# Kernel tuning notes

Measured on AMD Instinct MI355X. Metric: run time of the kernel, lower is better.

## Reference

```python
import jax, jax.numpy as jnp
import numpy as np

TOP_K = 2


def setup_inputs() -> dict:
    key = jax.random.key(0)
    ks = jax.random.split(key, 5)
    B, S, D, F, E = 2, 2048, 1024, 3584, 8
    scale_in = 1.0 / np.sqrt(D)
    scale_f = 1.0 / np.sqrt(F)
    return {
        "hidden_states": jax.random.normal(ks[0], (B, S, D), dtype=jnp.float32),
        "gate_w": jax.random.normal(ks[1], (E, D), dtype=jnp.float32) * scale_in,
        "w1": jax.random.normal(ks[2], (E, F, D), dtype=jnp.float32) * scale_in,
        "w3": jax.random.normal(ks[3], (E, F, D), dtype=jnp.float32) * scale_in,
        "w2": jax.random.normal(ks[4], (E, D, F), dtype=jnp.float32) * scale_f,
    }


def _routing_weights(logits):
    # softmax over experts, select top-k, renormalize (Mixtral semantics)
    probs = jax.nn.softmax(logits, axis=-1)          # [T, E]
    topv, topi = jax.lax.top_k(probs, TOP_K)          # [T, k]
    topv = topv / jnp.sum(topv, axis=-1, keepdims=True)
    T, E = logits.shape
    w = jnp.zeros((T, E), dtype=logits.dtype)
    w = w.at[jnp.arange(T)[:, None], topi].set(topv)  # dense [T, E] routing weights
    return w


def reference(hidden_states, gate_w, w1, w3, w2):
    B, S, D = hidden_states.shape
    x = hidden_states.reshape(-1, D)                  # [T, D]
    logits = x @ gate_w.T                             # [T, E]
    rw = _routing_weights(logits)                     # [T, E]
    E = gate_w.shape[0]
    out = jnp.zeros_like(x)
    for e in range(E):                                # fixed small expert count
        h = jax.nn.silu(x @ w1[e].T) * (x @ w3[e].T)  # [T, F]
        out = out + rw[:, e:e + 1] * (h @ w2[e].T)    # [T, D]
    return out.reshape(B, S, D)
```

## Files before the change

### kernel.cpp

```cpp
#include <hip/hip_runtime.h>
#include <hip/hip_bf16.h>


#define T_TOK 4096
#define DIM   1024
#define FF    3584
#define NE    8
#define BM    128
#define CAP   (T_TOK*2 + NE*BM)

#define OFF_TOPI   256UL
#define OFF_TOPW   33024UL
#define OFF_TOKPOS 65792UL
#define OFF_ROWTOK 98560UL
#define OFF_XB     135424UL
#define OFF_BIG    8524032UL
#define OFF_W2B    OFF_BIG
#define OFF_RES    (OFF_BIG + 58720256UL)
#define OFF_H      (OFF_BIG + 117440512UL)
#define WS_NEED    (OFF_H + 66060288UL)

using f32x4 = __attribute__((ext_vector_type(4))) float;
using s16x8 = __attribute__((ext_vector_type(8))) short;

__device__ __forceinline__ ushort f2b(float f) {
    __hip_bfloat16 b = __float2bfloat16(f);
    ushort u; __builtin_memcpy(&u, &b, 2); return u;
}
__device__ __forceinline__ float blo(uint u){ u <<= 16; float f; __builtin_memcpy(&f,&u,4); return f; }
__device__ __forceinline__ float bhi(uint u){ u &= 0xFFFF0000u; float f; __builtin_memcpy(&f,&u,4); return f; }

__device__ __forceinline__ void gl_lds16(const ushort* g, ushort* l) {
    __builtin_amdgcn_global_load_lds(
        (const __attribute__((address_space(1))) void*)g,
        (__attribute__((address_space(3))) void*)l, 16, 0, 0);
}
__device__ __forceinline__ uint4 pack8(float4 v0, float4 v1) {
    uint4 o;
    o.x = f2b(v0.x) | ((uint)f2b(v0.y) << 16);
    o.y = f2b(v0.z) | ((uint)f2b(v0.w) << 16);
    o.z = f2b(v1.x) | ((uint)f2b(v1.y) << 16);
    o.w = f2b(v1.z) | ((uint)f2b(v1.w) << 16);
    return o;
}

#define LGKM0 do { asm volatile("s_waitcnt lgkmcnt(0)" ::: "memory"); \
                   __builtin_amdgcn_sched_barrier(0); } while (0)
#define VMC(n) asm volatile("s_waitcnt vmcnt(" #n ")" ::: "memory")
#define BAR()  __builtin_amdgcn_s_barrier()

__global__ __launch_bounds__(256)
void k_route(const float* __restrict__ x, const float* __restrict__ gw,
             int* __restrict__ topi, float* __restrict__ topw, int* __restrict__ counts)
{
    __shared__ float gws[NE*DIM];
    const int tid = threadIdx.x;
    for (int i = tid; i < NE*DIM/4; i += 256)
        ((float4*)gws)[i] = ((const float4*)gw)[i];
    __syncthreads();

    const int lane = tid & 63, wid = tid >> 6;
    const int t = blockIdx.x*4 + wid;

    float4 xr[4];
    const float4* xrow = (const float4*)(x + (size_t)t*DIM) + lane*4;
    #pragma unroll
    for (int i = 0; i < 4; ++i) xr[i] = xrow[i];

    float lg[NE];
    #pragma unroll
    for (int e = 0; e < NE; ++e) {
        const float4* g4 = (const float4*)(gws + e*DIM) + lane*4;
        float s = 0.f;
        #pragma unroll
        for (int i = 0; i < 4; ++i) {
            float4 g = g4[i];
            s += xr[i].x*g.x + xr[i].y*g.y + xr[i].z*g.z + xr[i].w*g.w;
        }
        #pragma unroll
        for (int off = 32; off; off >>= 1) s += __shfl_xor(s, off);
        lg[e] = s;
    }
    if (lane == 0) {
        float b1 = -1e30f, b2 = -1e30f; int i1 = 0, i2 = 0;
        #pragma unroll
        for (int e = 0; e < NE; ++e) {
            float v = lg[e];
            if (v > b1)      { b2 = b1; i2 = i1; b1 = v; i1 = e; }
            else if (v > b2) { b2 = v; i2 = e; }
        }
        float p2 = __expf(b2 - b1);
        float inv = 1.f / (1.f + p2);
        topi[2*t]   = i1; topi[2*t+1] = i2;
        topw[2*t]   = inv; topw[2*t+1] = p2*inv;
        atomicAdd(&counts[i1], 1); atomicAdd(&counts[i2], 1);
    }
}

__global__ void k_scan(const int* __restrict__ counts, int* __restrict__ offs,
                       int* __restrict__ rowTok)
{
    if (threadIdx.x == 0) {
        int acc = 0; offs[0] = 0;
        for (int e = 0; e < NE; ++e) {
            int p = (counts[e] + BM - 1) & ~(BM - 1);
            acc += p; offs[e+1] = acc;
        }
    }
    for (int i = threadIdx.x; i < CAP; i += blockDim.x) rowTok[i] = -1;
}

__global__ __launch_bounds__(256)
void k_scatter(const int* __restrict__ topi,
               const int* __restrict__ offs, int* __restrict__ cursor,
               int* __restrict__ rowTok, int* __restrict__ tokPos)
{
    int t = blockIdx.x*256 + threadIdx.x;
    #pragma unroll
    for (int j = 0; j < 2; ++j) {
        int e = topi[2*t + j];
        int pos = offs[e] + atomicAdd(&cursor[e], 1);
        rowTok[pos] = t;
        tokPos[2*t + j] = pos;
    }
}

__global__ __launch_bounds__(256)
void k_cvt(const float* __restrict__ src, ushort* __restrict__ dst)
{
    size_t i = (size_t)blockIdx.x*256 + threadIdx.x;
    float4 v0 = ((const float4*)src)[2*i], v1 = ((const float4*)src)[2*i+1];
    ((uint4*)dst)[i] = pack8(v0, v1);
}

__global__ __launch_bounds__(256)
void k_cvt13(const float* __restrict__ w1, const float* __restrict__ w3,
             ushort* __restrict__ w13)
{
    int i = blockIdx.x*256 + threadIdx.x;
    int k8 = i & 127;
    int rd = i >> 7;
    int e   = rd / 7168;
    int rem = rd - e*7168;
    int pb  = rem >> 9;
    int sc  = rem & 511;
    int g = sc >> 6, half = (sc >> 5) & 1, c = sc & 31;
    int f = pb*256 + g*32 + c;
    const float* src = (half ? w3 : w1) + ((size_t)e*FF + f)*DIM + k8*8;
    float4 v0 = ((const float4*)src)[0], v1 = ((const float4*)src)[1];
    ((uint4*)w13)[i] = pack8(v0, v1);
}

__global__ __launch_bounds__(512)
void k_gemm1(const ushort* __restrict__ xb, const ushort* __restrict__ w13,
             const int* __restrict__ offs, const int* __restrict__ rowTok,
             ushort* __restrict__ hout)
{
    __shared__ __align__(16) ushort As[3][128*32];
    __shared__ __align__(16) ushort Bs[3][512*32];
    const int rowStart = blockIdx.y * BM;
    if (rowStart >= offs[8]) return;
    int e = 0;
    #pragma unroll
    for (int k = 1; k < NE; ++k) if (rowStart >= offs[k]) e = k;
    const int pb = blockIdx.x;
    const ushort* __restrict__ Wb = w13 + ((size_t)(e*14 + pb)) * 512 * DIM;

    const int tid = threadIdx.x;
    const int lane = tid & 63, wid = tid >> 6;
    const int lo = lane & 15, hi = lane >> 4;

    const int srow = tid >> 2;
    const int q    = tid & 3;
    const int sig  = (tid >> 3) & 3;
    int tokS = rowTok[rowStart + srow]; if (tokS < 0) tokS = 0;
    const ushort* aS = xb + (size_t)tokS*DIM + (q ^ sig)*8;
    const ushort* bS = Wb + (size_t)srow*DIM + (q ^ sig)*8;

    const int sig2  = (lo >> 1) & 3;
    const int rdA   = lo*32 + ((hi ^ sig2) * 8);
    const int rdB   = (wid*64 + lo)*32 + ((hi ^ sig2) * 8);

    f32x4 acc[8][4];
    #pragma unroll
    for (int m = 0; m < 8; ++m)
        #pragma unroll
        for (int n = 0; n < 4; ++n) acc[m][n] = (f32x4)(0.f);

    #pragma unroll
    for (int t0 = 0; t0 < 2; ++t0) {
        gl_lds16(aS + t0*32, &As[t0][0] + wid*512);
        #pragma unroll
        for (int j = 0; j < 4; ++j)
            gl_lds16(bS + (size_t)j*(128*DIM) + t0*32, &Bs[t0][0] + j*4096 + wid*512);
    }
    VMC(5);
    BAR();

    int cur = 0, nxt = 2;
    const int NK = DIM/32;
    for (int t = 0; t < NK; ++t) {
        const ushort* Ab = &As[cur][0];
        const ushort* Bb = &Bs[cur][0];
        const bool pf = (t + 2 < NK);
        s16x8 a[4], b[4];
        #pragma unroll
        for (int n = 0; n < 4; ++n) b[n] = *(const s16x8*)(Bb + n*512 + rdB);
        #pragma unroll
        for (int m = 0; m < 4; ++m) a[m] = *(const s16x8*)(Ab + m*512 + rdA);
        if (pf) {
            gl_lds16(aS + (t+2)*32, &As[nxt][0] + wid*512);
            gl_lds16(bS + (t+2)*32,                 &Bs[nxt][0] + wid*512);
            gl_lds16(bS + (size_t)(128*DIM) + (t+2)*32, &Bs[nxt][0] + 4096 + wid*512);
        }
        BAR();
        LGKM0;
        __builtin_amdgcn_s_setprio(1);
        #pragma unroll
        for (int m = 0; m < 4; ++m)
            #pragma unroll
            for (int n = 0; n < 4; ++n)
                acc[m][n] = __builtin_amdgcn_mfma_f32_16x16x32_bf16(a[m], b[n], acc[m][n], 0, 0, 0);
        __builtin_amdgcn_s_setprio(0);
        BAR();
        #pragma unroll
        for (int m = 0; m < 4; ++m) a[m] = *(const s16x8*)(Ab + 2048 + m*512 + rdA);
        if (pf) {
            gl_lds16(bS + (size_t)(256*DIM) + (t+2)*32, &Bs[nxt][0] + 8192  + wid*512);
            gl_lds16(bS + (size_t)(384*DIM) + (t+2)*32, &Bs[nxt][0] + 12288 + wid*512);
        }
        BAR();
        LGKM0;
        __builtin_amdgcn_s_setprio(1);
        #pragma unroll
        for (int m = 0; m < 4; ++m)
            #pragma unroll
            for (int n = 0; n < 4; ++n)
                acc[4+m][n] = __builtin_amdgcn_mfma_f32_16x16x32_bf16(a[m], b[n], acc[4+m][n], 0, 0, 0);
        __builtin_amdgcn_s_setprio(0);
        if (t == NK-2) { VMC(0); } else { VMC(5); }
        BAR();
        cur = (cur == 2) ? 0 : cur + 1;
        nxt = (nxt == 2) ? 0 : nxt + 1;
    }

    const int fbase = pb*256 + wid*32;
    #pragma unroll
    for (int m = 0; m < 8; ++m)
        #pragma unroll
        for (int n = 0; n < 2; ++n) {
            f32x4 v1 = acc[m][n], v3 = acc[m][n+2];
            int f = fbase + n*16 + lo;
            #pragma unroll
            for (int j = 0; j < 4; ++j) {
                int row = m*16 + hi*4 + j;
                float s = v1[j];
                float val = (s / (1.f + __expf(-s))) * v3[j];
                hout[(size_t)(rowStart + row)*FF + f] = f2b(val);
            }
        }
}

__global__ __launch_bounds__(512)
void k_gemm2(const ushort* __restrict__ h, const ushort* __restrict__ w2b,
             const int* __restrict__ offs, ushort* __restrict__ res)
{
    __shared__ __align__(16) ushort As[3][128*32];
    __shared__ __align__(16) ushort Bs[3][256*32];
    const int rowStart = blockIdx.y * BM;
    if (rowStart >= offs[8]) return;
    int e = 0;
    #pragma unroll
    for (int k = 1; k < NE; ++k) if (rowStart >= offs[k]) e = k;
    const int dc = blockIdx.x * 256;
    const ushort* __restrict__ W2 = w2b + ((size_t)e*DIM + dc)*FF;

    const int tid = threadIdx.x;
    const int lane = tid & 63, wid = tid >> 6;
    const int wr = wid >> 2, wc = wid & 3;
    const int lo = lane & 15, hi = lane >> 4;

    const int srow = tid >> 2;
    const int q    = tid & 3;
    const int sig  = (tid >> 3) & 3;
    const ushort* aS = h  + (size_t)(rowStart + srow)*FF + (q ^ sig)*8;
    const ushort* bS = W2 + (size_t)srow*FF + (q ^ sig)*8;

    const int sig2 = (lo >> 1) & 3;
    const int rdA  = (wr*64 + lo)*32 + ((hi ^ sig2) * 8);
    const int rdB  = (wc*64 + lo)*32 + ((hi ^ sig2) * 8);

    f32x4 acc[4][4];
    #pragma unroll
    for (int m = 0; m < 4; ++m)
        #pragma unroll
        for (int n = 0; n < 4; ++n) acc[m][n] = (f32x4)(0.f);

    #pragma unroll
    for (int t0 = 0; t0 < 2; ++t0) {
        gl_lds16(aS + t0*32, &As[t0][0] + wid*512);
        #pragma unroll
        for (int j = 0; j < 2; ++j)
            gl_lds16(bS + (size_t)j*(128*FF) + t0*32, &Bs[t0][0] + j*4096 + wid*512);
    }
    VMC(3);
    BAR();

    int cur = 0, nxt = 2;
    const int NK = FF/32;
    for (int t = 0; t < NK; ++t) {
        const ushort* Ab = &As[cur][0];
        const ushort* Bb = &Bs[cur][0];
        const bool pf = (t + 2 < NK);
        s16x8 a[4], b[4];
        #pragma unroll
        for (int n = 0; n < 4; ++n) b[n] = *(const s16x8*)(Bb + n*512 + rdB);
        #pragma unroll
        for (int m = 0; m < 4; ++m) a[m] = *(const s16x8*)(Ab + m*512 + rdA);
        if (pf) {
            gl_lds16(aS + (t+2)*32, &As[nxt][0] + wid*512);
            gl_lds16(bS + (t+2)*32,                &Bs[nxt][0] + wid*512);
            gl_lds16(bS + (size_t)(128*FF) + (t+2)*32, &Bs[nxt][0] + 4096 + wid*512);
        }
        BAR();
        LGKM0;
        __builtin_amdgcn_s_setprio(1);
        #pragma unroll
        for (int m = 0; m < 4; ++m)
            #pragma unroll
            for (int n = 0; n < 4; ++n)
                acc[m][n] = __builtin_amdgcn_mfma_f32_16x16x32_bf16(a[m], b[n], acc[m][n], 0, 0, 0);
        __builtin_amdgcn_s_setprio(0);
        if (t == NK-2) { VMC(0); } else { VMC(3); }
        BAR();
        cur = (cur == 2) ? 0 : cur + 1;
        nxt = (nxt == 2) ? 0 : nxt + 1;
    }

    #pragma unroll
    for (int m = 0; m < 4; ++m)
        #pragma unroll
        for (int j = 0; j < 4; ++j) {
            int prow = rowStart + wr*64 + m*16 + hi*4 + j;
            #pragma unroll
            for (int n = 0; n < 4; ++n) {
                int d = dc + wc*64 + n*16 + lo;
                res[(size_t)prow*DIM + d] = f2b(acc[m][n][j]);
            }
        }
}

__global__ __launch_bounds__(256)
void k_combine(const ushort* __restrict__ res, const int* __restrict__ tokPos,
               const float* __restrict__ topw, float* __restrict__ out)
{
    int i = blockIdx.x*256 + threadIdx.x;
    int t = i >> 7;
    int g = i & 127;
    int pA = tokPos[2*t], pB = tokPos[2*t+1];
    float wA = topw[2*t], wB = topw[2*t+1];
    uint4 a = *(const uint4*)(res + (size_t)pA*DIM + g*8);
    uint4 b = *(const uint4*)(res + (size_t)pB*DIM + g*8);
    float4 o0, o1;
    o0.x = wA*blo(a.x) + wB*blo(b.x);  o0.y = wA*bhi(a.x) + wB*bhi(b.x);
    o0.z = wA*blo(a.y) + wB*blo(b.y);  o0.w = wA*bhi(a.y) + wB*bhi(b.y);
    o1.x = wA*blo(a.z) + wB*blo(b.z);  o1.y = wA*bhi(a.z) + wB*bhi(b.z);
    o1.z = wA*blo(a.w) + wB*blo(b.w);  o1.w = wA*bhi(a.w) + wB*bhi(b.w);
    float4* dst = (float4*)(out + (size_t)t*DIM + g*8);
    dst[0] = o0; dst[1] = o1;
}

extern "C" void kernel_launch(void* const* d_in, const int* in_sizes, int n_in,
                              void* d_out, int out_size, void* d_ws, size_t ws_size,
                              hipStream_t stream)
{
    const float* x  = (const float*)d_in[0];
    const float* gw = (const float*)d_in[1];
    const float* w1 = (const float*)d_in[2];
    const float* w3 = (const float*)d_in[3];
    const float* w2 = (const float*)d_in[4];
    float* out = (float*)d_out;
    char* ws = (char*)d_ws;
    if (ws_size < WS_NEED) return;

    int*    counts = (int*)ws;
    int*    cursor = counts + 8;
    int*    offs   = counts + 16;
    int*    topi   = (int*)  (ws + OFF_TOPI);
    float*  topw   = (float*)(ws + OFF_TOPW);
    int*    tokPos = (int*)  (ws + OFF_TOKPOS);
    int*    rowTok = (int*)  (ws + OFF_ROWTOK);
    ushort* xb     = (ushort*)(ws + OFF_XB);
    ushort* w13b   = (ushort*)(ws + OFF_BIG);
    ushort* w2b    = (ushort*)(ws + OFF_W2B);
    ushort* res    = (ushort*)(ws + OFF_RES);
    ushort* h      = (ushort*)(ws + OFF_H);

    hipMemsetAsync(ws, 0, 256, stream);

    k_route  <<<T_TOK/4, 256, 0, stream>>>(x, gw, topi, topw, counts);
    k_scan   <<<1, 256, 0, stream>>>(counts, offs, rowTok);
    k_scatter<<<T_TOK/256, 256, 0, stream>>>(topi, offs, cursor, rowTok, tokPos);
    k_cvt    <<<(T_TOK*DIM/8)/256, 256, 0, stream>>>(x, xb);
    k_cvt13  <<<(2*NE*FF*DIM/8)/256, 256, 0, stream>>>(w1, w3, w13b);
    k_gemm1  <<<dim3(14, CAP/BM), 512, 0, stream>>>(xb, w13b, offs, rowTok, h);
    k_cvt    <<<(NE*DIM*FF/8)/256, 256, 0, stream>>>(w2, w2b);
    k_gemm2  <<<dim3(DIM/256, CAP/BM), 512, 0, stream>>>(h, w2b, offs, res);
    k_combine<<<(T_TOK*DIM/8)/256, 256, 0, stream>>>(res, tokPos, topw, out);
}
```

Measured before the change: 539.5 us.

## Retile MoE GEMMs and fuse combine into gemm2 via atomic scatter-add

Expert row padding rises to 256. gemm1 becomes a 256-row by 128-column (w1/w3 interleaved) tile with 256 threads and two blocks per CU, and gemm2 becomes 128x128 tiles with three blocks per CU. The separate combine kernel and the bf16 result buffer are removed: gemm2 scales each row by its routing weight and atomically adds fp32 into the zeroed output. The bf16 copy of x is staged in the output buffer before the memset. This trades a combine pass and intermediate traffic for atomic contention, nondeterministic summation order and extra padded rows.

```diff
diff --git a/kernel.cpp b/kernel.cpp
--- a/kernel.cpp
+++ b/kernel.cpp
@@ -6,19 +6,16 @@
 #define DIM   1024
 #define FF    3584
 #define NE    8
-#define BM    128
-#define CAP   (T_TOK*2 + NE*BM)
+#define CAP   (T_TOK*2 + NE*256)
 
 #define OFF_TOPI   256UL
 #define OFF_TOPW   33024UL
-#define OFF_TOKPOS 65792UL
-#define OFF_ROWTOK 98560UL
-#define OFF_XB     135424UL
-#define OFF_BIG    8524032UL
-#define OFF_W2B    OFF_BIG
-#define OFF_RES    (OFF_BIG + 58720256UL)
-#define OFF_H      (OFF_BIG + 117440512UL)
-#define WS_NEED    (OFF_H + 66060288UL)
+#define OFF_ROWTOK 65792UL
+#define OFF_ROWW   106752UL
+#define OFF_W13    147712UL
+#define OFF_W2B    OFF_W13
+#define OFF_H      (OFF_W13 + 117440512UL)
+#define WS_NEED    (OFF_H + 73400320UL)
 
 using f32x4 = __attribute__((ext_vector_type(4))) float;
 using s16x8 = __attribute__((ext_vector_type(8))) short;
@@ -27,9 +24,6 @@
     __hip_bfloat16 b = __float2bfloat16(f);
     ushort u; __builtin_memcpy(&u, &b, 2); return u;
 }
-__device__ __forceinline__ float blo(uint u){ u <<= 16; float f; __builtin_memcpy(&f,&u,4); return f; }
-__device__ __forceinline__ float bhi(uint u){ u &= 0xFFFF0000u; float f; __builtin_memcpy(&f,&u,4); return f; }
-
 __device__ __forceinline__ void gl_lds16(const ushort* g, ushort* l) {
     __builtin_amdgcn_global_load_lds(
         (const __attribute__((address_space(1))) void*)g,
@@ -103,7 +97,7 @@
     if (threadIdx.x == 0) {
         int acc = 0; offs[0] = 0;
         for (int e = 0; e < NE; ++e) {
-            int p = (counts[e] + BM - 1) & ~(BM - 1);
+            int p = (counts[e] + 255) & ~255;
             acc += p; offs[e+1] = acc;
         }
     }
@@ -111,9 +105,9 @@
 }
 
 __global__ __launch_bounds__(256)
-void k_scatter(const int* __restrict__ topi,
+void k_scatter(const int* __restrict__ topi, const float* __restrict__ topw,
                const int* __restrict__ offs, int* __restrict__ cursor,
-               int* __restrict__ rowTok, int* __restrict__ tokPos)
+               int* __restrict__ rowTok, float* __restrict__ rowW)
 {
     int t = blockIdx.x*256 + threadIdx.x;
     #pragma unroll
@@ -121,7 +115,7 @@
         int e = topi[2*t + j];
         int pos = offs[e] + atomicAdd(&cursor[e], 1);
         rowTok[pos] = t;
-        tokPos[2*t + j] = pos;
+        rowW[pos] = topw[2*t + j];
     }
 }
 
@@ -139,47 +133,57 @@
 {
     int i = blockIdx.x*256 + threadIdx.x;
     int k8 = i & 127;
-    int rd = i >> 7;
-    int e   = rd / 7168;
-    int rem = rd - e*7168;
-    int pb  = rem >> 9;
-    int sc  = rem & 511;
-    int g = sc >> 6, half = (sc >> 5) & 1, c = sc & 31;
-    int f = pb*256 + g*32 + c;
-    const float* src = (half ? w3 : w1) + ((size_t)e*FF + f)*DIM + k8*8;
+    int r  = i >> 7;
+    int rd = r & 127;
+    int sb = (r >> 7) % 56;
+    int e  = r / 7168;
+    int f  = sb*64 + (rd >> 5)*16 + (rd & 15);
+    const float* src = (((rd >> 4) & 1) ? w3 : w1) + ((size_t)e*FF + f)*DIM + k8*8;
     float4 v0 = ((const float4*)src)[0], v1 = ((const float4*)src)[1];
     ((uint4*)w13)[i] = pack8(v0, v1);
 }
 
-__global__ __launch_bounds__(512)
+#define G1_SLOT 12288
+__global__ __launch_bounds__(256, 2)
 void k_gemm1(const ushort* __restrict__ xb, const ushort* __restrict__ w13,
              const int* __restrict__ offs, const int* __restrict__ rowTok,
              ushort* __restrict__ hout)
 {
-    __shared__ __align__(16) ushort As[3][128*32];
-    __shared__ __align__(16) ushort Bs[3][512*32];
-    const int rowStart = blockIdx.y * BM;
+    __shared__ __align__(16) ushort L[3*G1_SLOT];
+    const int rowStart = blockIdx.y * 256;
     if (rowStart >= offs[8]) return;
     int e = 0;
     #pragma unroll
     for (int k = 1; k < NE; ++k) if (rowStart >= offs[k]) e = k;
-    const int pb = blockIdx.x;
-    const ushort* __restrict__ Wb = w13 + ((size_t)(e*14 + pb)) * 512 * DIM;
-
-    const int tid = threadIdx.x;
-    const int lane = tid & 63, wid = tid >> 6;
+    const int sb = blockIdx.x;
+    const ushort* __restrict__ Wb = w13 + (((size_t)e*56 + sb) * 128) * DIM;
+
+    const int tid = threadIdx.x, lane = tid & 63, wid = tid >> 6;
+    const int wr = wid >> 1, wc = wid & 1;
     const int lo = lane & 15, hi = lane >> 4;
 
-    const int srow = tid >> 2;
-    const int q    = tid & 3;
-    const int sig  = (tid >> 3) & 3;
-    int tokS = rowTok[rowStart + srow]; if (tokS < 0) tokS = 0;
-    const ushort* aS = xb + (size_t)tokS*DIM + (q ^ sig)*8;
-    const ushort* bS = Wb + (size_t)srow*DIM + (q ^ sig)*8;
-
-    const int sig2  = (lo >> 1) & 3;
-    const int rdA   = lo*32 + ((hi ^ sig2) * 8);
-    const int rdB   = (wid*64 + lo)*32 + ((hi ^ sig2) * 8);
+    const int srow = lane >> 2;
+    const int sch  = (lane & 3) ^ ((lane >> 3) & 3);
+    const ushort* aS[4];
+    #pragma unroll
+    for (int j = 0; j < 4; ++j) {
+        int tk = rowTok[rowStart + j*64 + wid*16 + srow]; if (tk < 0) tk = 0;
+        aS[j] = xb + (size_t)tk*DIM + sch*8;
+    }
+    const ushort* bS[2];
+    #pragma unroll
+    for (int j = 0; j < 2; ++j)
+        bS[j] = Wb + (size_t)(j*64 + wid*16 + srow)*DIM + sch*8;
+    ushort* const dA = L + wid*512;
+    ushort* const dB = L + 8192 + wid*512;
+
+    const int sig = (lo >> 1) & 3;
+    const int roff = ((hi ^ sig) * 8);
+    int rdA[8], rdB[4];
+    #pragma unroll
+    for (int m = 0; m < 8; ++m) rdA[m] = (wr*128 + m*16 + lo)*32 + roff;
+    #pragma unroll
+    for (int n = 0; n < 4; ++n) rdB[n] = 8192 + (wc*64 + n*16 + lo)*32 + roff;
 
     f32x4 acc[8][4];
     #pragma unroll
@@ -189,29 +193,28 @@
 
     #pragma unroll
     for (int t0 = 0; t0 < 2; ++t0) {
-        gl_lds16(aS + t0*32, &As[t0][0] + wid*512);
-        #pragma unroll
-        for (int j = 0; j < 4; ++j)
-            gl_lds16(bS + (size_t)j*(128*DIM) + t0*32, &Bs[t0][0] + j*4096 + wid*512);
-    }
-    VMC(5);
+        #pragma unroll
+        for (int j = 0; j < 4; ++j) gl_lds16(aS[j] + t0*32, dA + t0*G1_SLOT + j*2048);
+        #pragma unroll
+        for (int j = 0; j < 2; ++j) gl_lds16(bS[j] + t0*32, dB + t0*G1_SLOT + j*2048);
+    }
+    VMC(6);
     BAR();
 
+    const int NK = DIM/32;
     int cur = 0, nxt = 2;
-    const int NK = DIM/32;
     for (int t = 0; t < NK; ++t) {
-        const ushort* Ab = &As[cur][0];
-        const ushort* Bb = &Bs[cur][0];
+        const ushort* Lb = L + cur*G1_SLOT;
         const bool pf = (t + 2 < NK);
         s16x8 a[4], b[4];
         #pragma unroll
-        for (int n = 0; n < 4; ++n) b[n] = *(const s16x8*)(Bb + n*512 + rdB);
-        #pragma unroll
-        for (int m = 0; m < 4; ++m) a[m] = *(const s16x8*)(Ab + m*512 + rdA);
+        for (int n = 0; n < 4; ++n) b[n] = *(const s16x8*)(Lb + rdB[n]);
+        #pragma unroll
+        for (int m = 0; m < 4; ++m) a[m] = *(const s16x8*)(Lb + rdA[m]);
         if (pf) {
-            gl_lds16(aS + (t+2)*32, &As[nxt][0] + wid*512);
-            gl_lds16(bS + (t+2)*32,                 &Bs[nxt][0] + wid*512);
-            gl_lds16(bS + (size_t)(128*DIM) + (t+2)*32, &Bs[nxt][0] + 4096 + wid*512);
+            #pragma unroll
+            for (int j = 0; j < 3; ++j)
+                gl_lds16(aS[j] + (t+2)*32, dA + nxt*G1_SLOT + j*2048);
         }
         BAR();
         LGKM0;
@@ -224,10 +227,11 @@
         __builtin_amdgcn_s_setprio(0);
         BAR();
         #pragma unroll
-        for (int m = 0; m < 4; ++m) a[m] = *(const s16x8*)(Ab + 2048 + m*512 + rdA);
+        for (int m = 0; m < 4; ++m) a[m] = *(const s16x8*)(Lb + rdA[4+m]);
         if (pf) {
-            gl_lds16(bS + (size_t)(256*DIM) + (t+2)*32, &Bs[nxt][0] + 8192  + wid*512);
-            gl_lds16(bS + (size_t)(384*DIM) + (t+2)*32, &Bs[nxt][0] + 12288 + wid*512);
+            gl_lds16(aS[3] + (t+2)*32, dA + nxt*G1_SLOT + 3*2048);
+            gl_lds16(bS[0] + (t+2)*32, dB + nxt*G1_SLOT);
+            gl_lds16(bS[1] + (t+2)*32, dB + nxt*G1_SLOT + 2048);
         }
         BAR();
         LGKM0;
@@ -238,57 +242,67 @@
             for (int n = 0; n < 4; ++n)
                 acc[4+m][n] = __builtin_amdgcn_mfma_f32_16x16x32_bf16(a[m], b[n], acc[4+m][n], 0, 0, 0);
         __builtin_amdgcn_s_setprio(0);
-        if (t == NK-2) { VMC(0); } else { VMC(5); }
+        if (t < NK-2) { VMC(6); } else { VMC(0); }
         BAR();
         cur = (cur == 2) ? 0 : cur + 1;
         nxt = (nxt == 2) ? 0 : nxt + 1;
     }
 
-    const int fbase = pb*256 + wid*32;
     #pragma unroll
     for (int m = 0; m < 8; ++m)
         #pragma unroll
-        for (int n = 0; n < 2; ++n) {
-            f32x4 v1 = acc[m][n], v3 = acc[m][n+2];
-            int f = fbase + n*16 + lo;
+        for (int p = 0; p < 2; ++p) {
+            f32x4 v1 = acc[m][2*p], v3 = acc[m][2*p+1];
+            int f = sb*64 + (wc*2 + p)*16 + lo;
             #pragma unroll
             for (int j = 0; j < 4; ++j) {
-                int row = m*16 + hi*4 + j;
+                int row = rowStart + wr*128 + m*16 + hi*4 + j;
                 float s = v1[j];
                 float val = (s / (1.f + __expf(-s))) * v3[j];
-                hout[(size_t)(rowStart + row)*FF + f] = f2b(val);
+                hout[(size_t)row*FF + f] = f2b(val);
             }
         }
 }
 
-__global__ __launch_bounds__(512)
+#define G2_SLOT 8192
+__global__ __launch_bounds__(256, 3)
 void k_gemm2(const ushort* __restrict__ h, const ushort* __restrict__ w2b,
-             const int* __restrict__ offs, ushort* __restrict__ res)
-{
-    __shared__ __align__(16) ushort As[3][128*32];
-    __shared__ __align__(16) ushort Bs[3][256*32];
-    const int rowStart = blockIdx.y * BM;
+             const int* __restrict__ offs, const int* __restrict__ rowTok,
+             const float* __restrict__ rowW, float* __restrict__ out)
+{
+    __shared__ __align__(16) ushort L[3*G2_SLOT];
+    const int rowStart = blockIdx.y * 128;
     if (rowStart >= offs[8]) return;
     int e = 0;
     #pragma unroll
     for (int k = 1; k < NE; ++k) if (rowStart >= offs[k]) e = k;
-    const int dc = blockIdx.x * 256;
+    const int dc = blockIdx.x * 128;
     const ushort* __restrict__ W2 = w2b + ((size_t)e*DIM + dc)*FF;
 
-    const int tid = threadIdx.x;
-    const int lane = tid & 63, wid = tid >> 6;
-    const int wr = wid >> 2, wc = wid & 3;
+    const int tid = threadIdx.x, lane = tid & 63, wid = tid >> 6;
+    const int wr = wid >> 1, wc = wid & 1;
     const int lo = lane & 15, hi = lane >> 4;
 
-    const int srow = tid >> 2;
-    const int q    = tid & 3;
-    const int sig  = (tid >> 3) & 3;
-    const ushort* aS = h  + (size_t)(rowStart + srow)*FF + (q ^ sig)*8;
-    const ushort* bS = W2 + (size_t)srow*FF + (q ^ sig)*8;
-
-    const int sig2 = (lo >> 1) & 3;
-    const int rdA  = (wr*64 + lo)*32 + ((hi ^ sig2) * 8);
-    const int rdB  = (wc*64 + lo)*32 + ((hi ^ sig2) * 8);
+    const int srow = lane >> 2;
+    const int sch  = (lane & 3) ^ ((lane >> 3) & 3);
+    const ushort* aS[2];
+    const ushort* bS[2];
+    #pragma unroll
+    for (int j = 0; j < 2; ++j) {
+        int r = j*64 + wid*16 + srow;
+        aS[j] = h  + (size_t)(rowStart + r)*FF + sch*8;
+        bS[j] = W2 + (size_t)r*FF + sch*8;
+    }
+    ushort* const dA = L + wid*512;
+    ushort* const dB = L + 4096 + wid*512;
+
+    const int sig = (lo >> 1) & 3;
+    const int roff = ((hi ^ sig) * 8);
+    int rdA[4], rdB[4];
+    #pragma unroll
+    for (int m = 0; m < 4; ++m) rdA[m] = (wr*64 + m*16 + lo)*32 + roff;
+    #pragma unroll
+    for (int n = 0; n < 4; ++n) rdB[n] = 4096 + (wc*64 + n*16 + lo)*32 + roff;
 
     f32x4 acc[4][4];
     #pragma unroll
@@ -298,29 +312,29 @@
 
     #pragma unroll
     for (int t0 = 0; t0 < 2; ++t0) {
-        gl_lds16(aS + t0*32, &As[t0][0] + wid*512);
-        #pragma unroll
-        for (int j = 0; j < 2; ++j)
-            gl_lds16(bS + (size_t)j*(128*FF) + t0*32, &Bs[t0][0] + j*4096 + wid*512);
-    }
-    VMC(3);
+        #pragma unroll
+        for (int j = 0; j < 2; ++j) gl_lds16(aS[j] + t0*32, dA + t0*G2_SLOT + j*2048);
+        #pragma unroll
+        for (int j = 0; j < 2; ++j) gl_lds16(bS[j] + t0*32, dB + t0*G2_SLOT + j*2048);
+    }
+    VMC(4);
     BAR();
 
+    const int NK = FF/32;
     int cur = 0, nxt = 2;
-    const int NK = FF/32;
     for (int t = 0; t < NK; ++t) {
-        const ushort* Ab = &As[cur][0];
-        const ushort* Bb = &Bs[cur][0];
+        const ushort* Lb = L + cur*G2_SLOT;
         const bool pf = (t + 2 < NK);
         s16x8 a[4], b[4];
         #pragma unroll
-        for (int n = 0; n < 4; ++n) b[n] = *(const s16x8*)(Bb + n*512 + rdB);
-        #pragma unroll
-        for (int m = 0; m < 4; ++m) a[m] = *(const s16x8*)(Ab + m*512 + rdA);
+        for (int n = 0; n < 4; ++n) b[n] = *(const s16x8*)(Lb + rdB[n]);
+        #pragma unroll
+        for (int m = 0; m < 4; ++m) a[m] = *(const s16x8*)(Lb + rdA[m]);
         if (pf) {
-            gl_lds16(aS + (t+2)*32, &As[nxt][0] + wid*512);
-            gl_lds16(bS + (t+2)*32,                &Bs[nxt][0] + wid*512);
-            gl_lds16(bS + (size_t)(128*FF) + (t+2)*32, &Bs[nxt][0] + 4096 + wid*512);
+            #pragma unroll
+            for (int j = 0; j < 2; ++j) gl_lds16(aS[j] + (t+2)*32, dA + nxt*G2_SLOT + j*2048);
+            #pragma unroll
+            for (int j = 0; j < 2; ++j) gl_lds16(bS[j] + (t+2)*32, dB + nxt*G2_SLOT + j*2048);
         }
         BAR();
         LGKM0;
@@ -331,7 +345,7 @@
             for (int n = 0; n < 4; ++n)
                 acc[m][n] = __builtin_amdgcn_mfma_f32_16x16x32_bf16(a[m], b[n], acc[m][n], 0, 0, 0);
         __builtin_amdgcn_s_setprio(0);
-        if (t == NK-2) { VMC(0); } else { VMC(3); }
+        if (t < NK-2) { VMC(4); } else { VMC(0); }
         BAR();
         cur = (cur == 2) ? 0 : cur + 1;
         nxt = (nxt == 2) ? 0 : nxt + 1;
@@ -342,32 +356,15 @@
         #pragma unroll
         for (int j = 0; j < 4; ++j) {
             int prow = rowStart + wr*64 + m*16 + hi*4 + j;
+            int tok = rowTok[prow];
+            if (tok < 0) continue;
+            float w = rowW[prow];
             #pragma unroll
             for (int n = 0; n < 4; ++n) {
                 int d = dc + wc*64 + n*16 + lo;
-                res[(size_t)prow*DIM + d] = f2b(acc[m][n][j]);
+                atomicAdd(&out[(size_t)tok*DIM + d], w * acc[m][n][j]);
             }
         }
-}
-
-__global__ __launch_bounds__(256)
-void k_combine(const ushort* __restrict__ res, const int* __restrict__ tokPos,
-               const float* __restrict__ topw, float* __restrict__ out)
-{
-    int i = blockIdx.x*256 + threadIdx.x;
-    int t = i >> 7;
-    int g = i & 127;
-    int pA = tokPos[2*t], pB = tokPos[2*t+1];
-    float wA = topw[2*t], wB = topw[2*t+1];
-    uint4 a = *(const uint4*)(res + (size_t)pA*DIM + g*8);
-    uint4 b = *(const uint4*)(res + (size_t)pB*DIM + g*8);
-    float4 o0, o1;
-    o0.x = wA*blo(a.x) + wB*blo(b.x);  o0.y = wA*bhi(a.x) + wB*bhi(b.x);
-    o0.z = wA*blo(a.y) + wB*blo(b.y);  o0.w = wA*bhi(a.y) + wB*bhi(b.y);
-    o1.x = wA*blo(a.z) + wB*blo(b.z);  o1.y = wA*bhi(a.z) + wB*bhi(b.z);
-    o1.z = wA*blo(a.w) + wB*blo(b.w);  o1.w = wA*bhi(a.w) + wB*bhi(b.w);
-    float4* dst = (float4*)(out + (size_t)t*DIM + g*8);
-    dst[0] = o0; dst[1] = o1;
 }
 
 extern "C" void kernel_launch(void* const* d_in, const int* in_sizes, int n_in,
@@ -388,23 +385,22 @@
     int*    offs   = counts + 16;
     int*    topi   = (int*)  (ws + OFF_TOPI);
     float*  topw   = (float*)(ws + OFF_TOPW);
-    int*    tokPos = (int*)  (ws + OFF_TOKPOS);
     int*    rowTok = (int*)  (ws + OFF_ROWTOK);
-    ushort* xb     = (ushort*)(ws + OFF_XB);
-    ushort* w13b   = (ushort*)(ws + OFF_BIG);
+    float*  rowW   = (float*)(ws + OFF_ROWW);
+    ushort* w13b   = (ushort*)(ws + OFF_W13);
     ushort* w2b    = (ushort*)(ws + OFF_W2B);
-    ushort* res    = (ushort*)(ws + OFF_RES);
     ushort* h      = (ushort*)(ws + OFF_H);
+    ushort* xb     = (ushort*)d_out;
 
     hipMemsetAsync(ws, 0, 256, stream);
 
     k_route  <<<T_TOK/4, 256, 0, stream>>>(x, gw, topi, topw, counts);
     k_scan   <<<1, 256, 0, stream>>>(counts, offs, rowTok);
-    k_scatter<<<T_TOK/256, 256, 0, stream>>>(topi, offs, cursor, rowTok, tokPos);
+    k_scatter<<<T_TOK/256, 256, 0, stream>>>(topi, topw, offs, cursor, rowTok, rowW);
     k_cvt    <<<(T_TOK*DIM/8)/256, 256, 0, stream>>>(x, xb);
     k_cvt13  <<<(2*NE*FF*DIM/8)/256, 256, 0, stream>>>(w1, w3, w13b);
-    k_gemm1  <<<dim3(14, CAP/BM), 512, 0, stream>>>(xb, w13b, offs, rowTok, h);
+    k_gemm1  <<<dim3(56, CAP/256), 256, 0, stream>>>(xb, w13b, offs, rowTok, h);
     k_cvt    <<<(NE*DIM*FF/8)/256, 256, 0, stream>>>(w2, w2b);
-    k_gemm2  <<<dim3(DIM/256, CAP/BM), 512, 0, stream>>>(h, w2b, offs, res);
-    k_combine<<<(T_TOK*DIM/8)/256, 256, 0, stream>>>(res, tokPos, topw, out);
-}
+    hipMemsetAsync(d_out, 0, (size_t)T_TOK*DIM*4, stream);
+    k_gemm2  <<<dim3(DIM/128, CAP/128), 256, 0, stream>>>(h, w2b, offs, rowTok, rowW, out);
+}
```

New measurement: 514.3 us. 4.7% less time.
